# Optimization experiments

Measured on AMD Instinct MI355X. Metric: run time of the kernel, lower is better.

Reference implementation:

```python
import jax, jax.numpy as jnp
import numpy as np

NUM_HEADS = 16


def setup_inputs() -> dict:
    key = jax.random.key(0)
    ks = jax.random.split(key, 6)
    B, S, D = 2, 2048, 2048
    scale = 0.02
    return {
        "hidden_states": jax.random.normal(ks[0], (B, S, D), dtype=jnp.float32),
        "Wq": jax.random.normal(ks[1], (D, D), dtype=jnp.float32) * scale,
        "Wk": jax.random.normal(ks[2], (D, D), dtype=jnp.float32) * scale,
        "Wv": jax.random.normal(ks[3], (D, D), dtype=jnp.float32) * scale,
        "Wo": jax.random.normal(ks[4], (D, D), dtype=jnp.float32) * scale,
        "bo": jnp.zeros((D,), dtype=jnp.float32),
    }


def reference(hidden_states, Wq, Wk, Wv, Wo, bo):
    B, S, D = hidden_states.shape
    H = NUM_HEADS
    hd = D // H

    def split_heads(t):  # [B,S,D] -> [B,H,S,hd]
        return t.reshape(B, S, H, hd).transpose(0, 2, 1, 3)

    q = split_heads(hidden_states @ Wq)
    k = split_heads(hidden_states @ Wk)
    v = split_heads(hidden_states @ Wv)

    # Note: GPT-Neo does NOT scale by 1/sqrt(head_dim); scores computed in fp32.
    scores = jnp.einsum("bhqd,bhkd->bhqk", q.astype(jnp.float32), k.astype(jnp.float32))
    causal = jnp.tril(jnp.ones((S, S), dtype=bool))  # [S,S], True = attend
    mask_value = jnp.finfo(jnp.float32).min
    scores = jnp.where(causal[None, None, :, :], scores, mask_value)
    attn = jax.nn.softmax(scores, axis=-1).astype(v.dtype)

    ctx = jnp.einsum("bhqk,bhkd->bhqd", attn, v)  # [B,H,S,hd]
    ctx = ctx.transpose(0, 2, 1, 3).reshape(B, S, D)  # merge heads
    out = ctx @ Wo + bo
    return out
```

## Files before the change

### kernel.cpp

```cpp
#include <hip/hip_runtime.h>
#include <hip/hip_bf16.h>
#include <math.h>

#define BATCH 2
#define SEQ   2048
#define DDIM  2048
#define NH    16
#define HD    128
#define MROWS (BATCH * SEQ)

typedef unsigned short u16;
typedef __bf16 bf16x8 __attribute__((ext_vector_type(8)));
typedef float  f32x4  __attribute__((ext_vector_type(4)));

__device__ __forceinline__ u16 f2bf(float f) {
  unsigned int u = __float_as_uint(f);
  u += 0x7fffu + ((u >> 16) & 1u);
  return (u16)(u >> 16);
}
__device__ __forceinline__ float bf2f(u16 h) {
  return __uint_as_float(((unsigned int)h) << 16);
}

__device__ __forceinline__ void gload16(const void* g, void* s) {
  __builtin_amdgcn_global_load_lds((const __attribute__((address_space(1))) void*)g,
                                   (__attribute__((address_space(3))) void*)s, 16, 0, 0);
}

__global__ void split_x(const float* __restrict__ in, u16* __restrict__ hi,
                        u16* __restrict__ lo) {
  const int i = blockIdx.x * blockDim.x + threadIdx.x;
  float4 v = ((const float4*)in)[i];
  ushort4 h, l;
  h.x = f2bf(v.x); l.x = f2bf(v.x - bf2f(h.x));
  h.y = f2bf(v.y); l.y = f2bf(v.y - bf2f(h.y));
  h.z = f2bf(v.z); l.z = f2bf(v.z - bf2f(h.z));
  h.w = f2bf(v.w); l.w = f2bf(v.w - bf2f(h.w));
  ((ushort4*)hi)[i] = h;
  ((ushort4*)lo)[i] = l;
}

__global__ void transpose_w(const float* __restrict__ W, u16* __restrict__ Wth,
                            u16* __restrict__ Wtl) {
  __shared__ float t[32][33];
  const int tx = threadIdx.x, ty = threadIdx.y;
  const int c0 = blockIdx.x * 32, r0 = blockIdx.y * 32;
#pragma unroll
  for (int i = 0; i < 4; ++i)
    t[ty + i * 8][tx] = W[(size_t)(r0 + ty + i * 8) * DDIM + c0 + tx];
  __syncthreads();
#pragma unroll
  for (int i = 0; i < 4; ++i) {
    const float v = t[tx][ty + i * 8];
    const u16 h = f2bf(v);
    const size_t idx = (size_t)(c0 + ty + i * 8) * DDIM + r0 + tx;
    Wth[idx] = h;
    if (Wtl) Wtl[idx] = f2bf(v - bf2f(h));
  }
}

__global__ void transpose_v(const u16* __restrict__ V, u16* __restrict__ Vt) {
  __shared__ u16 t[32][33];
  const int tx = threadIdx.x, ty = threadIdx.y;
  const int s0 = blockIdx.x * 32;
  const int d0 = blockIdx.y * 32;
  const int bh = blockIdx.z;
  const int b = bh >> 4, h = bh & 15;
#pragma unroll
  for (int i = 0; i < 4; ++i)
    t[ty + i * 8][tx] = V[(size_t)(b * SEQ + s0 + ty + i * 8) * DDIM + h * HD + d0 + tx];
  __syncthreads();
#pragma unroll
  for (int i = 0; i < 4; ++i)
    Vt[((size_t)bh * HD + d0 + ty + i * 8) * SEQ + s0 + tx] = t[tx][ty + i * 8];
}

template <int MODE>
__global__ __launch_bounds__(256)
void gemm_kernel(const u16* __restrict__ A, const u16* __restrict__ Bt,
                 void* __restrict__ Cout, const float* __restrict__ bias) {
  constexpr int K = DDIM, N = DDIM;
  __shared__ __align__(16) u16 As[128 * 64];
  __shared__ __align__(16) u16 Bs[128 * 64];
  const int tid = threadIdx.x;
  const int wave = tid >> 6;
  const int lane = tid & 63;
  const int lr = lane & 15, lg = lane >> 4;
  const int bm = blockIdx.y * 128, bn = blockIdx.x * 128;
  const int wr = wave >> 1, wc = wave & 1;

  f32x4 acc[4][4] = {};

  const int srow = wave * 32 + (lane >> 3);
  const int scol = (lane & 7) * 8;
  const u16* Ag = A  + (size_t)(bm + srow) * K + scol;
  const u16* Bg = Bt + (size_t)(bn + srow) * K + scol;

  for (int k0 = 0; k0 < K; k0 += 64) {
    __syncthreads();
#pragma unroll
    for (int it = 0; it < 4; ++it) {
      gload16(Ag + (size_t)it * 8 * K + k0, &As[(wave * 32 + it * 8) * 64]);
      gload16(Bg + (size_t)it * 8 * K + k0, &Bs[(wave * 32 + it * 8) * 64]);
    }
    __syncthreads();
#pragma unroll
    for (int kk = 0; kk < 64; kk += 32) {
      bf16x8 af[4], bfr[4];
#pragma unroll
      for (int i = 0; i < 4; ++i)
        af[i] = *(const bf16x8*)&As[(wr * 64 + i * 16 + lr) * 64 + kk + lg * 8];
#pragma unroll
      for (int j = 0; j < 4; ++j)
        bfr[j] = *(const bf16x8*)&Bs[(wc * 64 + j * 16 + lr) * 64 + kk + lg * 8];
#pragma unroll
      for (int i = 0; i < 4; ++i)
#pragma unroll
        for (int j = 0; j < 4; ++j)
          acc[i][j] = __builtin_amdgcn_mfma_f32_16x16x32_bf16(af[i], bfr[j], acc[i][j], 0, 0, 0);
    }
  }

#pragma unroll
  for (int i = 0; i < 4; ++i) {
    const int row0 = bm + wr * 64 + i * 16 + lg * 4;
#pragma unroll
    for (int j = 0; j < 4; ++j) {
      const int col = bn + wc * 64 + j * 16 + lr;
#pragma unroll
      for (int e = 0; e < 4; ++e) {
        const int row = row0 + e;
        const float v = acc[i][j][e];
        if constexpr (MODE == 0) {
          ((u16*)Cout)[(size_t)row * N + col] = f2bf(v);
        } else {
          ((float*)Cout)[(size_t)row * N + col] = v + bias[col];
        }
      }
    }
  }
}

template <bool WRITE_LO>
__global__ __launch_bounds__(256)
void gemm3_kernel(const u16* __restrict__ Ah, const u16* __restrict__ Al,
                  const u16* __restrict__ Bh, const u16* __restrict__ Bl,
                  u16* __restrict__ Ch, u16* __restrict__ Cl) {
  constexpr int K = DDIM, N = DDIM;
  __shared__ __align__(16) u16 Ash[128 * 64];
  __shared__ __align__(16) u16 Asl[128 * 64];
  __shared__ __align__(16) u16 Bsh[128 * 64];
  __shared__ __align__(16) u16 Bsl[128 * 64];
  const int tid = threadIdx.x;
  const int wave = tid >> 6;
  const int lane = tid & 63;
  const int lr = lane & 15, lg = lane >> 4;
  const int bm = blockIdx.y * 128, bn = blockIdx.x * 128;
  const int wr = wave >> 1, wc = wave & 1;

  f32x4 acc[4][4] = {};

  const int srow = wave * 32 + (lane >> 3);
  const int scol = (lane & 7) * 8;
  const size_t aoff = (size_t)(bm + srow) * K + scol;
  const size_t boff = (size_t)(bn + srow) * K + scol;

  for (int k0 = 0; k0 < K; k0 += 64) {
    __syncthreads();
#pragma unroll
    for (int it = 0; it < 4; ++it) {
      const size_t ro = (size_t)it * 8 * K + k0;
      const int ls = (wave * 32 + it * 8) * 64;
      gload16(Ah + aoff + ro, &Ash[ls]);
      gload16(Al + aoff + ro, &Asl[ls]);
      gload16(Bh + boff + ro, &Bsh[ls]);
      gload16(Bl + boff + ro, &Bsl[ls]);
    }
    __syncthreads();
#pragma unroll
    for (int kk = 0; kk < 64; kk += 32) {
      bf16x8 ah[4], al[4], bh[4], bl[4];
#pragma unroll
      for (int i = 0; i < 4; ++i) {
        const int off = (wr * 64 + i * 16 + lr) * 64 + kk + lg * 8;
        ah[i] = *(const bf16x8*)&Ash[off];
        al[i] = *(const bf16x8*)&Asl[off];
      }
#pragma unroll
      for (int j = 0; j < 4; ++j) {
        const int off = (wc * 64 + j * 16 + lr) * 64 + kk + lg * 8;
        bh[j] = *(const bf16x8*)&Bsh[off];
        bl[j] = *(const bf16x8*)&Bsl[off];
      }
#pragma unroll
      for (int i = 0; i < 4; ++i)
#pragma unroll
        for (int j = 0; j < 4; ++j) {
          acc[i][j] = __builtin_amdgcn_mfma_f32_16x16x32_bf16(ah[i], bh[j], acc[i][j], 0, 0, 0);
          acc[i][j] = __builtin_amdgcn_mfma_f32_16x16x32_bf16(ah[i], bl[j], acc[i][j], 0, 0, 0);
          acc[i][j] = __builtin_amdgcn_mfma_f32_16x16x32_bf16(al[i], bh[j], acc[i][j], 0, 0, 0);
        }
    }
  }

#pragma unroll
  for (int i = 0; i < 4; ++i) {
    const int row0 = bm + wr * 64 + i * 16 + lg * 4;
#pragma unroll
    for (int j = 0; j < 4; ++j) {
      const int col = bn + wc * 64 + j * 16 + lr;
#pragma unroll
      for (int e = 0; e < 4; ++e) {
        const float v = acc[i][j][e];
        const u16 h = f2bf(v);
        const size_t idx = (size_t)(row0 + e) * N + col;
        Ch[idx] = h;
        if constexpr (WRITE_LO) Cl[idx] = f2bf(v - bf2f(h));
      }
    }
  }
}

__global__ __launch_bounds__(256)
void attn_kernel(const u16* __restrict__ Qh, const u16* __restrict__ Khp,
                 const u16* __restrict__ Klp, const u16* __restrict__ Vt,
                 u16* __restrict__ ctx) {
  __shared__ __align__(16) u16 Ksh[2][32 * 128];
  __shared__ __align__(16) u16 Ksl[2][32 * 128];
  __shared__ __align__(16) u16 Vs [2][128 * 32];
  __shared__ __align__(16) u16 P_lds[4][16 * 32];
  const int tid = threadIdx.x;
  const int wave = tid >> 6, lane = tid & 63;
  const int lr = lane & 15, lg = lane >> 4;

  const int id = blockIdx.y * 32 + blockIdx.x;
  const int nid = (id & 7) * 128 + (id >> 3);
  const int bh = nid >> 5;
  const int qb = 31 - (nid & 31);
  const int q0 = qb * 64;
  const int b = bh >> 4, h = bh & 15;
  const int qw = q0 + wave * 16;
  const float NEG_INF = -__builtin_inff();

  const u16* Kg = Khp + (size_t)b * SEQ * DDIM + h * HD;
  const u16* Lg = Klp + (size_t)b * SEQ * DDIM + h * HD;
  const u16* Vg = Vt + (size_t)bh * HD * SEQ;

  bf16x8 qf[4];
#pragma unroll
  for (int kk = 0; kk < 4; ++kk)
    qf[kk] = *(const bf16x8*)&Qh[(size_t)(b * SEQ + qw + lr) * DDIM + h * HD + kk * 32 + lg * 8];

  const int krow0 = wave * 4 + (lane >> 4);
  const int kcolb = (lane & 15) << 4;
  const int vrow0 = wave * 16 + (lane >> 2);
  const int vcolb = (lane & 3) << 4;

  auto STAGE = [&](int buf, int t) {
    const int kbase = t * 32;
#pragma unroll
    for (int it = 0; it < 2; ++it) {
      const int r = it * 16 + krow0;
      const int c = (kcolb ^ ((r & 7) << 4)) >> 1;
      const size_t g = (size_t)(kbase + r) * DDIM + c;
      gload16(Kg + g, &Ksh[buf][it * 2048 + wave * 512]);
      gload16(Lg + g, &Ksl[buf][it * 2048 + wave * 512]);
    }
#pragma unroll
    for (int it = 0; it < 2; ++it) {
      const int d = it * 64 + vrow0;
      const int c = (vcolb ^ ((d & 3) << 4)) >> 1;
      gload16(Vg + (size_t)d * SEQ + kbase + c, &Vs[buf][it * 2048 + wave * 512]);
    }
  };

  float m[4], l[4];
#pragma unroll
  for (int e = 0; e < 4; ++e) { m[e] = NEG_INF; l[e] = 0.f; }
  f32x4 o[8] = {};

  const int nt = 2 * qb + 2;
  int cur = 0;
  STAGE(0, 0);
  __syncthreads();

  for (int t = 0; t < nt; ++t) {
    if (t + 1 < nt) STAGE(cur ^ 1, t + 1);
    const int k0 = t * 32;
    if (k0 <= qw + 15) {
      f32x4 s[2] = {};
#pragma unroll
      for (int fc = 0; fc < 2; ++fc) {
        const int r = fc * 16 + lr;
        const int sw = (r & 7) << 4;
#pragma unroll
        for (int kk = 0; kk < 4; ++kk) {
          const int idx = r * 128 + (((kk * 64 + lg * 16) ^ sw) >> 1);
          bf16x8 kfh = *(const bf16x8*)&Ksh[cur][idx];
          bf16x8 kfl = *(const bf16x8*)&Ksl[cur][idx];
          s[fc] = __builtin_amdgcn_mfma_f32_16x16x32_bf16(qf[kk], kfh, s[fc], 0, 0, 0);
          s[fc] = __builtin_amdgcn_mfma_f32_16x16x32_bf16(qf[kk], kfl, s[fc], 0, 0, 0);
        }
      }
#pragma unroll
      for (int e = 0; e < 4; ++e) {
        const int row = qw + lg * 4 + e;
#pragma unroll
        for (int fc = 0; fc < 2; ++fc) {
          const int key = k0 + fc * 16 + lr;
          if (key > row) s[fc][e] = NEG_INF;
        }
        float rm = fmaxf(s[0][e], s[1][e]);
        rm = fmaxf(rm, __shfl_xor(rm, 1));
        rm = fmaxf(rm, __shfl_xor(rm, 2));
        rm = fmaxf(rm, __shfl_xor(rm, 4));
        rm = fmaxf(rm, __shfl_xor(rm, 8));
        const float mn = fmaxf(m[e], rm);
        const float al = __expf(m[e] - mn);
        const float p0 = __expf(s[0][e] - mn);
        const float p1 = __expf(s[1][e] - mn);
        s[0][e] = p0; s[1][e] = p1;
        float rs = p0 + p1;
        rs += __shfl_xor(rs, 1);
        rs += __shfl_xor(rs, 2);
        rs += __shfl_xor(rs, 4);
        rs += __shfl_xor(rs, 8);
        l[e] = l[e] * al + rs;
        m[e] = mn;
#pragma unroll
        for (int db = 0; db < 8; ++db) o[db][e] *= al;
      }
#pragma unroll
      for (int fc = 0; fc < 2; ++fc)
#pragma unroll
        for (int e = 0; e < 4; ++e) {
          const int q = lg * 4 + e;
          const int kb = ((fc * 16 + lr) * 2) ^ ((q & 3) << 4);
          P_lds[wave][q * 32 + (kb >> 1)] = f2bf(s[fc][e]);
        }
      __builtin_amdgcn_wave_barrier();
      bf16x8 pf = *(const bf16x8*)&P_lds[wave][lr * 32 + (((lg * 16) ^ ((lr & 3) << 4)) >> 1)];
      __builtin_amdgcn_wave_barrier();
#pragma unroll
      for (int db = 0; db < 8; ++db) {
        const int d = db * 16 + lr;
        const int idx = d * 32 + (((lg * 16) ^ ((d & 3) << 4)) >> 1);
        bf16x8 vf = *(const bf16x8*)&Vs[cur][idx];
        o[db] = __builtin_amdgcn_mfma_f32_16x16x32_bf16(pf, vf, o[db], 0, 0, 0);
      }
    }
    __syncthreads();
    cur ^= 1;
  }

#pragma unroll
  for (int db = 0; db < 8; ++db)
#pragma unroll
    for (int e = 0; e < 4; ++e) {
      const float v = o[db][e] / l[e];
      ctx[(size_t)(b * SEQ + qw + lg * 4 + e) * DDIM + h * HD + db * 16 + lr] = f2bf(v);
    }
}

extern "C" void kernel_launch(void* const* d_in, const int* in_sizes, int n_in,
                              void* d_out, int out_size, void* d_ws, size_t ws_size,
                              hipStream_t stream) {
  const float* X  = (const float*)d_in[0];
  const float* Wq = (const float*)d_in[1];
  const float* Wk = (const float*)d_in[2];
  const float* Wv = (const float*)d_in[3];
  const float* Wo = (const float*)d_in[4];
  const float* bo = (const float*)d_in[5];
  float* out = (float*)d_out;

  const size_t SZ_XD = (size_t)MROWS * DDIM * 2;
  const size_t SZ_W  = (size_t)DDIM * DDIM * 2;

  char* p = (char*)d_ws;
  auto alloc = [&](size_t bytes) {
    char* r = p;
    p += (bytes + 255) & ~(size_t)255;
    return r;
  };
  u16* Xh  = (u16*)alloc(SZ_XD);
  u16* Xl  = (u16*)alloc(SZ_XD);
  u16* Wbh = (u16*)alloc(SZ_W);
  u16* Wbl = (u16*)alloc(SZ_W);
  u16* Qh  = (u16*)alloc(SZ_XD);
  u16* Kh  = (u16*)alloc(SZ_XD);
  u16* Kl  = (u16*)alloc(SZ_XD);
  u16* Vb  = (u16*)alloc(SZ_XD);
  u16* Vt  = Xh;
  u16* ctx = Qh;

  split_x<<<(MROWS * DDIM) / 1024, 256, 0, stream>>>(X, Xh, Xl);

  dim3 tb(32, 8);
  dim3 gg(DDIM / 128, MROWS / 128);

  transpose_w<<<dim3(64, 64), tb, 0, stream>>>(Wq, Wbh, Wbl);
  gemm3_kernel<false><<<gg, 256, 0, stream>>>(Xh, Xl, Wbh, Wbl, Qh, nullptr);

  transpose_w<<<dim3(64, 64), tb, 0, stream>>>(Wk, Wbh, Wbl);
  gemm3_kernel<true><<<gg, 256, 0, stream>>>(Xh, Xl, Wbh, Wbl, Kh, Kl);

  transpose_w<<<dim3(64, 64), tb, 0, stream>>>(Wv, Wbh, nullptr);
  gemm_kernel<0><<<gg, 256, 0, stream>>>(Xh, Wbh, Vb, nullptr);

  transpose_v<<<dim3(SEQ / 32, HD / 32, BATCH * NH), tb, 0, stream>>>(Vb, Vt);

  transpose_w<<<dim3(64, 64), tb, 0, stream>>>(Wo, Wbh, nullptr);

  attn_kernel<<<dim3(32, 32), 256, 0, stream>>>(Qh, Kh, Kl, Vt, ctx);

  gemm_kernel<2><<<gg, 256, 0, stream>>>(ctx, Wbh, out, bo);
}
```

Before: 633.9 us.

## Enlarge attention tiles to 128 queries and 64 keys with lazy rescaling and MFMA row sums

The attention kernel moves to 512-thread blocks covering 128 query rows, staging 64-key K/V tiles per iteration, so each K/V load is shared by twice as many waves and there are fewer block-wide barriers. The online softmax now skips rescaling unless the running max grows by more than a threshold, computes the row sum with an MFMA against a ones vector instead of shuffle reductions, and only applies the causal mask on diagonal tiles. Wave priority is raised around the MFMA sections. The costs are larger LDS use and lower occupancy (launch bounds 512,1), bf16 rounding in the row sum, and a threshold-based rescale that could lose precision for large score jumps.

Result: faster. 611.3 us (-3.6%).

```diff
diff --git a/kernel.cpp b/kernel.cpp
--- a/kernel.cpp
+++ b/kernel.cpp
@@ -221,23 +221,23 @@
   }
 }
 
-__global__ __launch_bounds__(256)
+__global__ __launch_bounds__(512, 1)
 void attn_kernel(const u16* __restrict__ Qh, const u16* __restrict__ Khp,
                  const u16* __restrict__ Klp, const u16* __restrict__ Vt,
                  u16* __restrict__ ctx) {
-  __shared__ __align__(16) u16 Ksh[2][32 * 128];
-  __shared__ __align__(16) u16 Ksl[2][32 * 128];
-  __shared__ __align__(16) u16 Vs [2][128 * 32];
-  __shared__ __align__(16) u16 P_lds[4][16 * 32];
+  __shared__ __align__(16) u16 Ksh[2][64 * 128];
+  __shared__ __align__(16) u16 Ksl[2][64 * 128];
+  __shared__ __align__(16) u16 Vs [2][128 * 64];
+  __shared__ __align__(16) u16 P_lds[8][16 * 32];
   const int tid = threadIdx.x;
   const int wave = tid >> 6, lane = tid & 63;
   const int lr = lane & 15, lg = lane >> 4;
 
-  const int id = blockIdx.y * 32 + blockIdx.x;
-  const int nid = (id & 7) * 128 + (id >> 3);
-  const int bh = nid >> 5;
-  const int qb = 31 - (nid & 31);
-  const int q0 = qb * 64;
+  const int id = blockIdx.y * 16 + blockIdx.x;
+  const int nid = (id & 7) * 64 + (id >> 3);
+  const int bh = nid >> 4;
+  const int qb = 15 - (nid & 15);
+  const int q0 = qb * 128;
   const int b = bh >> 4, h = bh & 15;
   const int qw = q0 + wave * 16;
   const float NEG_INF = -__builtin_inff();
@@ -251,32 +251,37 @@
   for (int kk = 0; kk < 4; ++kk)
     qf[kk] = *(const bf16x8*)&Qh[(size_t)(b * SEQ + qw + lr) * DDIM + h * HD + kk * 32 + lg * 8];
 
+  bf16x8 ones;
+#pragma unroll
+  for (int i = 0; i < 8; ++i) ones[i] = (__bf16)1.0f;
+
   const int krow0 = wave * 4 + (lane >> 4);
   const int kcolb = (lane & 15) << 4;
-  const int vrow0 = wave * 16 + (lane >> 2);
-  const int vcolb = (lane & 3) << 4;
+  const int vrow0 = wave * 8 + (lane >> 3);
+  const int vcolb = (lane & 7) << 4;
 
   auto STAGE = [&](int buf, int t) {
-    const int kbase = t * 32;
+    const int kbase = t * 64;
 #pragma unroll
     for (int it = 0; it < 2; ++it) {
-      const int r = it * 16 + krow0;
+      const int r = it * 32 + krow0;
       const int c = (kcolb ^ ((r & 7) << 4)) >> 1;
       const size_t g = (size_t)(kbase + r) * DDIM + c;
-      gload16(Kg + g, &Ksh[buf][it * 2048 + wave * 512]);
-      gload16(Lg + g, &Ksl[buf][it * 2048 + wave * 512]);
+      gload16(Kg + g, &Ksh[buf][it * 4096 + wave * 512]);
+      gload16(Lg + g, &Ksl[buf][it * 4096 + wave * 512]);
     }
 #pragma unroll
     for (int it = 0; it < 2; ++it) {
       const int d = it * 64 + vrow0;
-      const int c = (vcolb ^ ((d & 3) << 4)) >> 1;
-      gload16(Vg + (size_t)d * SEQ + kbase + c, &Vs[buf][it * 2048 + wave * 512]);
+      const int c = (vcolb ^ ((d & 7) << 4)) >> 1;
+      gload16(Vg + (size_t)d * SEQ + kbase + c, &Vs[buf][it * 4096 + wave * 512]);
     }
   };
 
-  float m[4], l[4];
-#pragma unroll
-  for (int e = 0; e < 4; ++e) { m[e] = NEG_INF; l[e] = 0.f; }
+  float m[4];
+  f32x4 lsum = {};
+#pragma unroll
+  for (int e = 0; e < 4; ++e) m[e] = NEG_INF;
   f32x4 o[8] = {};
 
   const int nt = 2 * qb + 2;
@@ -286,67 +291,82 @@
 
   for (int t = 0; t < nt; ++t) {
     if (t + 1 < nt) STAGE(cur ^ 1, t + 1);
-    const int k0 = t * 32;
-    if (k0 <= qw + 15) {
-      f32x4 s[2] = {};
-#pragma unroll
-      for (int fc = 0; fc < 2; ++fc) {
-        const int r = fc * 16 + lr;
-        const int sw = (r & 7) << 4;
-#pragma unroll
-        for (int kk = 0; kk < 4; ++kk) {
-          const int idx = r * 128 + (((kk * 64 + lg * 16) ^ sw) >> 1);
-          bf16x8 kfh = *(const bf16x8*)&Ksh[cur][idx];
-          bf16x8 kfl = *(const bf16x8*)&Ksl[cur][idx];
-          s[fc] = __builtin_amdgcn_mfma_f32_16x16x32_bf16(qf[kk], kfh, s[fc], 0, 0, 0);
-          s[fc] = __builtin_amdgcn_mfma_f32_16x16x32_bf16(qf[kk], kfl, s[fc], 0, 0, 0);
-        }
-      }
-#pragma unroll
-      for (int e = 0; e < 4; ++e) {
-        const int row = qw + lg * 4 + e;
+#pragma unroll
+    for (int ks = 0; ks < 2; ++ks) {
+      const int k0 = t * 64 + ks * 32;
+      if (k0 <= qw + 15) {
+        f32x4 s[2] = {};
+        __builtin_amdgcn_s_setprio(1);
 #pragma unroll
         for (int fc = 0; fc < 2; ++fc) {
-          const int key = k0 + fc * 16 + lr;
-          if (key > row) s[fc][e] = NEG_INF;
-        }
-        float rm = fmaxf(s[0][e], s[1][e]);
-        rm = fmaxf(rm, __shfl_xor(rm, 1));
-        rm = fmaxf(rm, __shfl_xor(rm, 2));
-        rm = fmaxf(rm, __shfl_xor(rm, 4));
-        rm = fmaxf(rm, __shfl_xor(rm, 8));
-        const float mn = fmaxf(m[e], rm);
-        const float al = __expf(m[e] - mn);
-        const float p0 = __expf(s[0][e] - mn);
-        const float p1 = __expf(s[1][e] - mn);
-        s[0][e] = p0; s[1][e] = p1;
-        float rs = p0 + p1;
-        rs += __shfl_xor(rs, 1);
-        rs += __shfl_xor(rs, 2);
-        rs += __shfl_xor(rs, 4);
-        rs += __shfl_xor(rs, 8);
-        l[e] = l[e] * al + rs;
-        m[e] = mn;
-#pragma unroll
-        for (int db = 0; db < 8; ++db) o[db][e] *= al;
-      }
-#pragma unroll
-      for (int fc = 0; fc < 2; ++fc)
+          const int r = ks * 32 + fc * 16 + lr;
+          const int sw = (r & 7) << 4;
+#pragma unroll
+          for (int kk = 0; kk < 4; ++kk) {
+            const int idx = r * 128 + (((kk * 64 + lg * 16) ^ sw) >> 1);
+            bf16x8 kfh = *(const bf16x8*)&Ksh[cur][idx];
+            bf16x8 kfl = *(const bf16x8*)&Ksl[cur][idx];
+            s[fc] = __builtin_amdgcn_mfma_f32_16x16x32_bf16(qf[kk], kfh, s[fc], 0, 0, 0);
+            s[fc] = __builtin_amdgcn_mfma_f32_16x16x32_bf16(qf[kk], kfl, s[fc], 0, 0, 0);
+          }
+        }
+        __builtin_amdgcn_s_setprio(0);
+        if (k0 + 31 > qw) {
+#pragma unroll
+          for (int e = 0; e < 4; ++e) {
+            const int row = qw + lg * 4 + e;
+#pragma unroll
+            for (int fc = 0; fc < 2; ++fc) {
+              const int key = k0 + fc * 16 + lr;
+              if (key > row) s[fc][e] = NEG_INF;
+            }
+          }
+        }
+        float rm[4];
 #pragma unroll
         for (int e = 0; e < 4; ++e) {
+          float r0 = fmaxf(s[0][e], s[1][e]);
+          r0 = fmaxf(r0, __shfl_xor(r0, 1));
+          r0 = fmaxf(r0, __shfl_xor(r0, 2));
+          r0 = fmaxf(r0, __shfl_xor(r0, 4));
+          r0 = fmaxf(r0, __shfl_xor(r0, 8));
+          rm[e] = r0;
+        }
+        const float need = fmaxf(fmaxf(rm[0] - m[0], rm[1] - m[1]),
+                                 fmaxf(rm[2] - m[2], rm[3] - m[3]));
+        if (!__all(need <= 8.0f)) {
+#pragma unroll
+          for (int e = 0; e < 4; ++e) {
+            const float mn = fmaxf(m[e], rm[e]);
+            const float al = __expf(m[e] - mn);
+#pragma unroll
+            for (int db = 0; db < 8; ++db) o[db][e] *= al;
+            lsum[e] *= al;
+            m[e] = mn;
+          }
+        }
+#pragma unroll
+        for (int e = 0; e < 4; ++e) {
+          const float p0 = __expf(s[0][e] - m[e]);
+          const float p1 = __expf(s[1][e] - m[e]);
           const int q = lg * 4 + e;
-          const int kb = ((fc * 16 + lr) * 2) ^ ((q & 3) << 4);
-          P_lds[wave][q * 32 + (kb >> 1)] = f2bf(s[fc][e]);
-        }
-      __builtin_amdgcn_wave_barrier();
-      bf16x8 pf = *(const bf16x8*)&P_lds[wave][lr * 32 + (((lg * 16) ^ ((lr & 3) << 4)) >> 1)];
-      __builtin_amdgcn_wave_barrier();
-#pragma unroll
-      for (int db = 0; db < 8; ++db) {
-        const int d = db * 16 + lr;
-        const int idx = d * 32 + (((lg * 16) ^ ((d & 3) << 4)) >> 1);
-        bf16x8 vf = *(const bf16x8*)&Vs[cur][idx];
-        o[db] = __builtin_amdgcn_mfma_f32_16x16x32_bf16(pf, vf, o[db], 0, 0, 0);
+          const int sw = (q & 3) << 4;
+          P_lds[wave][q * 32 + ((((lr) * 2) ^ sw) >> 1)] = f2bf(p0);
+          P_lds[wave][q * 32 + ((((16 + lr) * 2) ^ sw) >> 1)] = f2bf(p1);
+        }
+        __builtin_amdgcn_wave_barrier();
+        bf16x8 pf = *(const bf16x8*)&P_lds[wave][lr * 32 + (((lg * 16) ^ ((lr & 3) << 4)) >> 1)];
+        __builtin_amdgcn_wave_barrier();
+        __builtin_amdgcn_s_setprio(1);
+#pragma unroll
+        for (int db = 0; db < 8; ++db) {
+          const int d = db * 16 + lr;
+          const int idx = d * 64 + (((ks * 64 + lg * 16) ^ ((d & 7) << 4)) >> 1);
+          bf16x8 vf = *(const bf16x8*)&Vs[cur][idx];
+          o[db] = __builtin_amdgcn_mfma_f32_16x16x32_bf16(pf, vf, o[db], 0, 0, 0);
+        }
+        lsum = __builtin_amdgcn_mfma_f32_16x16x32_bf16(pf, ones, lsum, 0, 0, 0);
+        __builtin_amdgcn_s_setprio(0);
       }
     }
     __syncthreads();
@@ -357,7 +377,7 @@
   for (int db = 0; db < 8; ++db)
 #pragma unroll
     for (int e = 0; e < 4; ++e) {
-      const float v = o[db][e] / l[e];
+      const float v = o[db][e] / lsum[e];
       ctx[(size_t)(b * SEQ + qw + lg * 4 + e) * DDIM + h * HD + db * 16 + lr] = f2bf(v);
     }
 }
@@ -411,7 +431,7 @@
 
   transpose_w<<<dim3(64, 64), tb, 0, stream>>>(Wo, Wbh, nullptr);
 
-  attn_kernel<<<dim3(32, 32), 256, 0, stream>>>(Qh, Kh, Kl, Vt, ctx);
+  attn_kernel<<<dim3(16, 32), 512, 0, stream>>>(Qh, Kh, Kl, Vt, ctx);
 
   gemm_kernel<2><<<gg, 256, 0, stream>>>(ctx, Wbh, out, bo);
 }
```
